# Kernel tuning notes

Measured on AMD Instinct MI355X. Metric: run time of the kernel, lower is better.

## Reference

```python
import jax, jax.numpy as jnp
import numpy as np

TAU = 1.1      # LIF membrane time constant
ALPHA = 4.0    # sigmoid surrogate sharpness (spikingjelly default)
EPS = 1e-5     # BatchNorm eps
SCALE = 0.125  # attention scale


def lif(x, v_th):
    # Single-step LIF, v init 0, decay_input=True: v = x / tau; spike = H(v - v_th)
    # Straight-through: forward heaviside, backward sigmoid surrogate derivative.
    u = x / TAU - v_th
    sg = jax.nn.sigmoid(ALPHA * u)
    return sg + jax.lax.stop_gradient((u >= 0.0).astype(x.dtype) - sg)


def bn(x, gamma, beta):
    # BatchNorm1d in training mode on [B, C, N]: stats over (B, N) per channel
    mean = jnp.mean(x, axis=(0, 2), keepdims=True)
    var = jnp.var(x, axis=(0, 2), keepdims=True)
    return gamma[None, :, None] * (x - mean) * jax.lax.rsqrt(var + EPS) + beta[None, :, None]


def conv1x1(w, x):
    # Conv1d kernel_size=1: pointwise channel mix, x: [B,C,N], w: [O,C]
    return jnp.einsum('oc,bcn->bon', w, x)


def setup_inputs() -> dict:
    key = jax.random.key(0)
    B, C, N = 32, 512, 1024
    ks = jax.random.split(key, 6)
    s = 1.0 / np.sqrt(C)
    inp = {"x": jax.random.normal(ks[0], (B, C, N), jnp.float32)}
    for name, k in zip(["q", "k", "v", "proj"], ks[1:5]):
        inp[name + "_w"] = jax.random.uniform(k, (C, C), jnp.float32, -s, s)
        inp[name + "_gamma"] = jnp.ones((C,), jnp.float32)
        inp[name + "_beta"] = jnp.zeros((C,), jnp.float32)
    inp["proj_b"] = jax.random.uniform(ks[5], (C,), jnp.float32, -s, s)
    return inp


def reference(x, q_w, q_gamma, q_beta, k_w, k_gamma, k_beta, v_w, v_gamma, v_beta,
              proj_w, proj_b, proj_gamma, proj_beta):
    # x: [B, C, N]
    q = lif(bn(conv1x1(q_w, x), q_gamma, q_beta), 1.0)  # [B,C,N] spikes
    k = lif(bn(conv1x1(k_w, x), k_gamma, k_beta), 1.0)
    v = lif(bn(conv1x1(v_w, x), v_gamma, v_beta), 1.0)
    # linear (softmax-free) attention: kv[c,d] = sum_n k[n,c] v[n,d]
    kv = jnp.einsum('bcn,bdn->bcd', k, v)               # [B,C,C]
    attn = jnp.einsum('bcn,bcd->bdn', q, kv) * SCALE    # [B,C,N] (already transposed back)
    attn = lif(attn, 0.5)
    out = conv1x1(proj_w, attn) + proj_b[None, :, None]
    return lif(bn(out, proj_gamma, proj_beta), 1.0)
```

## Files before the change

### kernel.cpp

```cpp
#include <hip/hip_runtime.h>
#include <cstddef>


#define CC 512
#define BB 32
#define NN 1024

typedef __attribute__((ext_vector_type(4))) float v4f;
typedef __attribute__((ext_vector_type(2))) float v2f;
typedef __attribute__((ext_vector_type(4))) int v4i;
typedef __attribute__((ext_vector_type(8))) int v8i;
typedef unsigned char uchar;
typedef unsigned long long ull;

__device__ __forceinline__ uchar f2e4s(float v) {
  const uchar s = (v < 0.f) ? 0x80 : 0x00;
  float a = fabsf(v);
  if (a >= 464.f) return s | 0x7E;
  if (a < 0.015625f) {
    int q = (int)rintf(a * 512.f);
    return s | (uchar)q;
  }
  const int e = (int)((__float_as_uint(a) >> 23) & 0xFF) - 126;
  const float scale = __uint_as_float((unsigned)(4 - e + 127) << 23);
  const int q = (int)rintf(a * scale);
  int code = ((e - 1 + 7) << 3) + (q - 8);
  if (code > 0x7E) code = 0x7E;
  return s | (uchar)code;
}
__device__ __forceinline__ float e42f(uchar b) {
  const int e = (b >> 3) & 15, m = b & 7;
  const float mag = e ? __uint_as_float((unsigned)((e + 120) << 23) | ((unsigned)m << 20))
                      : (float)m * 0.001953125f;
  return (b & 0x80) ? -mag : mag;
}

__device__ __forceinline__ unsigned pk4_fp8(float a0, float a1, float a2, float a3) {
#if __has_builtin(__builtin_amdgcn_cvt_pk_fp8_f32)
  int r = __builtin_amdgcn_cvt_pk_fp8_f32(a0, a1, 0, false);
  r = __builtin_amdgcn_cvt_pk_fp8_f32(a2, a3, r, true);
  return (unsigned)r;
#else
  return (unsigned)f2e4s(a0) | ((unsigned)f2e4s(a1) << 8) |
         ((unsigned)f2e4s(a2) << 16) | ((unsigned)f2e4s(a3) << 24);
#endif
}
__device__ __forceinline__ uchar enc1(float v) {
#if __has_builtin(__builtin_amdgcn_cvt_pk_fp8_f32)
  return (uchar)(__builtin_amdgcn_cvt_pk_fp8_f32(v, v, 0, false) & 0xFF);
#else
  return f2e4s(v);
#endif
}
template <bool HI>
__device__ __forceinline__ v2f dec2(int src) {
#if __has_builtin(__builtin_amdgcn_cvt_pk_f32_fp8)
  return __builtin_amdgcn_cvt_pk_f32_fp8(src, HI);
#else
  v2f r;
  const int s = HI ? (src >> 16) : src;
  r[0] = e42f((uchar)s);
  r[1] = e42f((uchar)(s >> 8));
  return r;
#endif
}

__device__ __forceinline__ void gload16(const void* g, void* l) {
  __builtin_amdgcn_global_load_lds(
      (const __attribute__((address_space(1))) unsigned int*)g,
      (__attribute__((address_space(3))) unsigned int*)l, 16, 0, 0);
}

__device__ __forceinline__ float2 chan_affine(const float* __restrict__ P, int c,
                                              float g, float bt) {
  const float* pc = P + (size_t)c * 16;
  float S = 0.f, Q = 0.f;
#pragma unroll
  for (int t = 0; t < 8; t++) { S += pc[2 * t]; Q += pc[2 * t + 1]; }
  const float mean = S * (1.f / 32768.f);
  const float var = fmaxf(Q * (1.f / 32768.f) - mean * mean, 0.f);
  const float rinv = 1.f / sqrtf(var + 1e-5f);
  const float a = g * rinv;
  return make_float2(a, bt - mean * a);
}

template <int EPI>
__global__ __launch_bounds__(256) void gemm8(const uchar* __restrict__ A,
                                             const uchar* __restrict__ B,
                                             uchar* __restrict__ Cout,
                                             const float* __restrict__ bias,
                                             int M, int N, int K,
                                             long sA, long sB, long sC) {
  __shared__ __align__(16) uchar lds[32768];
  const int b = blockIdx.z;
  const uchar* Ab = A + (size_t)b * sA;
  const uchar* Bb = B + (size_t)b * sB;
  const int m0 = blockIdx.y * 128, n0 = blockIdx.x * 128;
  const int tid = threadIdx.x;
  const int wave = tid >> 6, lane = tid & 63;
  const int lrow = lane & 15, lquad = lane >> 4;
  const int wr = wave >> 1, wc = wave & 1;

  v4f acc[4][4];
#pragma unroll
  for (int i = 0; i < 4; i++)
#pragma unroll
    for (int j = 0; j < 4; j++) acc[i][j] = (v4f)0.f;

  const uchar* gA0 = Ab + (size_t)(m0 + 32 * wave + lrow) * K + lquad * 32;
  const uchar* gA1 = gA0 + (size_t)16 * K;
  const uchar* gB0 = Bb + (size_t)(n0 + 32 * wave + lrow) * K + lquad * 32;
  const uchar* gB1 = gB0 + (size_t)16 * K;
  uchar* lA0 = lds + (2 * wave) * 2048;
  uchar* lA1 = lA0 + 2048;
  uchar* lB0 = lds + 16384 + (2 * wave) * 2048;
  uchar* lB1 = lB0 + 2048;

  for (int k0 = 0; k0 < K; k0 += 128) {
    gload16(gA0, lA0);
    gload16(gA0 + 16, lA0 + 1024);
    gload16(gA1, lA1);
    gload16(gA1 + 16, lA1 + 1024);
    gload16(gB0, lB0);
    gload16(gB0 + 16, lB0 + 1024);
    gload16(gB1, lB1);
    gload16(gB1 + 16, lB1 + 1024);
    gA0 += 128; gA1 += 128; gB0 += 128; gB1 += 128;
    __syncthreads();
    const uchar* ra = lds + (size_t)(4 * wr) * 2048 + 16 * lane;
    const uchar* rb = lds + 16384 + (size_t)(4 * wc) * 2048 + 16 * lane;
    v8i af[4], bf[4];
#pragma unroll
    for (int i = 0; i < 4; i++) {
      const v4i lo = *(const v4i*)(ra + i * 2048);
      const v4i hi = *(const v4i*)(ra + i * 2048 + 1024);
      af[i][0] = lo[0]; af[i][1] = lo[1]; af[i][2] = lo[2]; af[i][3] = lo[3];
      af[i][4] = hi[0]; af[i][5] = hi[1]; af[i][6] = hi[2]; af[i][7] = hi[3];
    }
#pragma unroll
    for (int j = 0; j < 4; j++) {
      const v4i lo = *(const v4i*)(rb + j * 2048);
      const v4i hi = *(const v4i*)(rb + j * 2048 + 1024);
      bf[j][0] = lo[0]; bf[j][1] = lo[1]; bf[j][2] = lo[2]; bf[j][3] = lo[3];
      bf[j][4] = hi[0]; bf[j][5] = hi[1]; bf[j][6] = hi[2]; bf[j][7] = hi[3];
    }
#pragma unroll
    for (int i = 0; i < 4; i++)
#pragma unroll
      for (int j = 0; j < 4; j++)
        acc[i][j] = __builtin_amdgcn_mfma_scale_f32_16x16x128_f8f6f4(
            af[i], bf[j], acc[i][j], 0, 0, 0, 127, 0, 127);
    __syncthreads();
  }

  if (EPI == 3) {
#pragma unroll
    for (int mi = 0; mi < 4; mi++)
#pragma unroll
      for (int r = 0; r < 4; r++) {
        const float bi = bias[m0 + 64 * wr + 16 * mi + lquad * 4 + r];
#pragma unroll
        for (int ni = 0; ni < 4; ni++) acc[mi][ni][r] += bi;
      }
  }

#pragma unroll
  for (int mi = 0; mi < 4; mi++) {
    const int row0 = m0 + 64 * wr + 16 * mi + lquad * 4;
#pragma unroll
    for (int ni = 0; ni < 4; ni++) {
      const int col = n0 + 64 * wc + 16 * ni + lrow;
      uchar* cp = Cout + (size_t)b * sC + (size_t)row0 * N + col;
      if (EPI == 1) {
#pragma unroll
        for (int r = 0; r < 4; r++) {
          const float u = (acc[mi][ni][r] * 0.125f) / 1.1f - 0.5f;
          cp[(size_t)r * N] = (u >= 0.f) ? (uchar)0x38 : (uchar)0;
        }
      } else {
        const unsigned pk = pk4_fp8(acc[mi][ni][0], acc[mi][ni][1],
                                    acc[mi][ni][2], acc[mi][ni][3]);
#pragma unroll
        for (int r = 0; r < 4; r++) cp[(size_t)r * N] = (uchar)(pk >> (8 * r));
      }
    }
  }
}

template <int EPI>
__global__ __launch_bounds__(512, 2) void gemm8p(const uchar* __restrict__ A,
                                                 const uchar* __restrict__ B,
                                                 uchar* __restrict__ Cout,
                                                 const float* __restrict__ bias,
                                                 int M, int N, int K,
                                                 long sA, long sB, long sC) {
  __shared__ __align__(16) uchar lds[131072];
  const int b = blockIdx.z;
  const uchar* Ab = A + (size_t)b * sA;
  const uchar* Bb = B + (size_t)b * sB;
  const int m0 = blockIdx.y * 256, n0 = blockIdx.x * 256;
  const int tid = threadIdx.x;
  const int wave = tid >> 6, lane = tid & 63;
  const int lrow = lane & 15, lquad = lane >> 4;
  const int wr = wave >> 2, wc = wave & 3;

  v4f acc[8][4];
#pragma unroll
  for (int i = 0; i < 8; i++)
#pragma unroll
    for (int j = 0; j < 4; j++) acc[i][j] = (v4f)0.f;

  const uchar* gA0 = Ab + (size_t)(m0 + 32 * wave + lrow) * K + lquad * 32;
  const uchar* gA1 = gA0 + (size_t)16 * K;
  const uchar* gB0 = Bb + (size_t)(n0 + 32 * wave + lrow) * K + lquad * 32;
  const uchar* gB1 = gB0 + (size_t)16 * K;

  const int NT = K >> 7;

#define SSA_STAGE_A(bufi)                                   \
  do {                                                      \
    uchar* la = lds + (bufi) * 65536 + (2 * wave) * 2048;   \
    gload16(gA0, la);                                       \
    gload16(gA0 + 16, la + 1024);                           \
    gload16(gA1, la + 2048);                                \
    gload16(gA1 + 16, la + 3072);                           \
  } while (0)
#define SSA_STAGE_B(bufi)                                   \
  do {                                                      \
    uchar* lb = lds + (bufi) * 65536 + 32768 + (2 * wave) * 2048; \
    gload16(gB0, lb);                                       \
    gload16(gB0 + 16, lb + 1024);                           \
    gload16(gB1, lb + 2048);                                \
    gload16(gB1 + 16, lb + 3072);                           \
  } while (0)

  SSA_STAGE_A(0);
  SSA_STAGE_B(0);
  gA0 += 128; gA1 += 128; gB0 += 128; gB1 += 128;
  asm volatile("s_waitcnt vmcnt(0)" ::: "memory");
  __builtin_amdgcn_s_barrier();

  for (int kt = 0; kt < NT; ++kt) {
    const int cur = kt & 1;
    const int nxt = cur ^ 1;
    const bool more = (kt + 1 < NT);
    const uchar* raA = lds + cur * 65536 + (8 * wr) * 2048 + 16 * lane;
    const uchar* raB = lds + cur * 65536 + 32768 + (4 * wc) * 2048 + 16 * lane;
    v8i bf[4];
#pragma unroll
    for (int p = 0; p < 4; ++p) {
      const uchar* ra = raA + (2 * p) * 2048;
      const v4i a0lo = *(const v4i*)(ra);
      const v4i a0hi = *(const v4i*)(ra + 1024);
      const v4i a1lo = *(const v4i*)(ra + 2048);
      const v4i a1hi = *(const v4i*)(ra + 3072);
      if (p == 0) {
#pragma unroll
        for (int j = 0; j < 4; ++j) {
          const v4i lo = *(const v4i*)(raB + j * 2048);
          const v4i hi = *(const v4i*)(raB + j * 2048 + 1024);
          bf[j][0] = lo[0]; bf[j][1] = lo[1]; bf[j][2] = lo[2]; bf[j][3] = lo[3];
          bf[j][4] = hi[0]; bf[j][5] = hi[1]; bf[j][6] = hi[2]; bf[j][7] = hi[3];
        }
        if (more) SSA_STAGE_A(nxt);
      }
      if (p == 1 && more) {
        SSA_STAGE_B(nxt);
        gA0 += 128; gA1 += 128; gB0 += 128; gB1 += 128;
      }
      __builtin_amdgcn_s_barrier();
      asm volatile("s_waitcnt lgkmcnt(0)" ::: "memory");
      __builtin_amdgcn_sched_barrier(0);
      __builtin_amdgcn_s_setprio(1);
      v8i af0, af1;
      af0[0] = a0lo[0]; af0[1] = a0lo[1]; af0[2] = a0lo[2]; af0[3] = a0lo[3];
      af0[4] = a0hi[0]; af0[5] = a0hi[1]; af0[6] = a0hi[2]; af0[7] = a0hi[3];
      af1[0] = a1lo[0]; af1[1] = a1lo[1]; af1[2] = a1lo[2]; af1[3] = a1lo[3];
      af1[4] = a1hi[0]; af1[5] = a1hi[1]; af1[6] = a1hi[2]; af1[7] = a1hi[3];
#pragma unroll
      for (int j = 0; j < 4; ++j) {
        acc[2 * p][j] = __builtin_amdgcn_mfma_scale_f32_16x16x128_f8f6f4(
            af0, bf[j], acc[2 * p][j], 0, 0, 0, 127, 0, 127);
        acc[2 * p + 1][j] = __builtin_amdgcn_mfma_scale_f32_16x16x128_f8f6f4(
            af1, bf[j], acc[2 * p + 1][j], 0, 0, 0, 127, 0, 127);
      }
      __builtin_amdgcn_s_setprio(0);
      if (p == 3 && more) asm volatile("s_waitcnt vmcnt(0)" ::: "memory");
      __builtin_amdgcn_s_barrier();
    }
  }
#undef SSA_STAGE_A
#undef SSA_STAGE_B

  if (EPI == 3) {
#pragma unroll
    for (int mi = 0; mi < 8; mi++)
#pragma unroll
      for (int r = 0; r < 4; r++) {
        const float bi = bias[m0 + 128 * wr + 16 * mi + lquad * 4 + r];
#pragma unroll
        for (int ni = 0; ni < 4; ni++) acc[mi][ni][r] += bi;
      }
  }

#pragma unroll
  for (int mi = 0; mi < 8; mi++) {
    const int row0 = m0 + 128 * wr + 16 * mi + lquad * 4;
#pragma unroll
    for (int ni = 0; ni < 4; ni++) {
      const int col = n0 + 64 * wc + 16 * ni + lrow;
      uchar* cp = Cout + (size_t)b * sC + (size_t)row0 * N + col;
      if (EPI == 1) {
#pragma unroll
        for (int r = 0; r < 4; r++) {
          const float u = (acc[mi][ni][r] * 0.125f) / 1.1f - 0.5f;
          cp[(size_t)r * N] = (u >= 0.f) ? (uchar)0x38 : (uchar)0;
        }
      } else {
        const unsigned pk = pk4_fp8(acc[mi][ni][0], acc[mi][ni][1],
                                    acc[mi][ni][2], acc[mi][ni][3]);
#pragma unroll
        for (int r = 0; r < 4; r++) cp[(size_t)r * N] = (uchar)(pk >> (8 * r));
      }
    }
  }
}

__global__ __launch_bounds__(256) void stats_part8_k(const uchar* __restrict__ in,
                                                     float* __restrict__ P,
                                                     long bstride) {
  const int part = blockIdx.x, c = blockIdx.y;
  const int tid = threadIdx.x;
  const int bi = part * 4 + (tid >> 6);
  const int lane = tid & 63;
  const uchar* p = in + (size_t)bi * bstride + (size_t)c * 1024 + lane * 16;
  const uint4 u = *(const uint4*)p;
  const int w4[4] = {(int)u.x, (int)u.y, (int)u.z, (int)u.w};
  float s = 0.f, s2 = 0.f;
#pragma unroll
  for (int t = 0; t < 4; t++) {
    const v2f a = dec2<false>(w4[t]);
    const v2f bb = dec2<true>(w4[t]);
    s += (a[0] + a[1]) + (bb[0] + bb[1]);
    s2 += a[0] * a[0] + a[1] * a[1] + bb[0] * bb[0] + bb[1] * bb[1];
  }
#pragma unroll
  for (int off = 32; off > 0; off >>= 1) {
    s += __shfl_down(s, off, 64);
    s2 += __shfl_down(s2, off, 64);
  }
  __shared__ float rs[4], rq[4];
  const int w = tid >> 6;
  if (lane == 0) { rs[w] = s; rq[w] = s2; }
  __syncthreads();
  if (tid == 0) {
    float2 o = make_float2(rs[0] + rs[1] + rs[2] + rs[3],
                           rq[0] + rq[1] + rq[2] + rq[3]);
    *(float2*)(P + (size_t)(c * 8 + part) * 2) = o;
  }
}

__global__ __launch_bounds__(256) void apply_all_k(const uchar* __restrict__ qkv8,
                                                   uchar* __restrict__ q8,
                                                   uchar* __restrict__ k8,
                                                   uchar* __restrict__ v8,
                                                   const float* __restrict__ P,
                                                   const float* __restrict__ qg, const float* __restrict__ qb,
                                                   const float* __restrict__ kg, const float* __restrict__ kb,
                                                   const float* __restrict__ vg, const float* __restrict__ vb) {
  const int bid = blockIdx.x;
  const int tid = threadIdx.x;
  if (bid < 16384) {
    __shared__ uchar tile[32][33];
    const int nb = bid & 31, cb = (bid >> 5) & 15, b = bid >> 9;
    const int n0 = nb * 32, c0 = cb * 32;
    const uchar* in = qkv8 + (size_t)b * (1536 * 1024);
    const int cl = tid >> 3;
    const int n4 = (tid & 7) * 4;
    const int c = c0 + cl;
    const float2 ab = chan_affine(P, c, qg[c], qb[c]);
    const unsigned w = *(const unsigned*)(in + (size_t)c * 1024 + n0 + n4);
    const v2f a = dec2<false>((int)w);
    const v2f bb = dec2<true>((int)w);
    tile[cl][n4 + 0] = (ab.x * a[0] + ab.y >= 1.1f) ? (uchar)0x38 : (uchar)0;
    tile[cl][n4 + 1] = (ab.x * a[1] + ab.y >= 1.1f) ? (uchar)0x38 : (uchar)0;
    tile[cl][n4 + 2] = (ab.x * bb[0] + ab.y >= 1.1f) ? (uchar)0x38 : (uchar)0;
    tile[cl][n4 + 3] = (ab.x * bb[1] + ab.y >= 1.1f) ? (uchar)0x38 : (uchar)0;
    __syncthreads();
    uchar* out = q8 + (size_t)b * (NN * CC);
    const int nl = tid >> 3;
    const int cq = (tid & 7) * 4;
    uchar4 v;
    v.x = tile[cq][nl]; v.y = tile[cq + 1][nl];
    v.z = tile[cq + 2][nl]; v.w = tile[cq + 3][nl];
    *(uchar4*)(out + (size_t)(n0 + nl) * CC + c0 + cq) = v;
  } else {
    const int t0 = bid - 16384;
    const int sec = t0 >> 13;
    const int blk = t0 & 8191;
    const size_t t = (size_t)blk * 256 + tid;
    const size_t i = t * 8;
    const int b = (int)(i >> 19);
    const int rem = (int)(i & 524287);
    const int c = rem >> 10, n = rem & 1023;
    const int cg = 512 + 512 * sec + c;
    const float2 ab = chan_affine(P, cg, sec ? vg[c] : kg[c], sec ? vb[c] : kb[c]);
    const uchar* src = qkv8 + (size_t)b * (1536 * 1024) + (size_t)cg * 1024 + n;
    const uint2 u = *(const uint2*)src;
    ull packed = 0;
    {
      const v2f a = dec2<false>((int)u.x);
      const v2f bb = dec2<true>((int)u.x);
      const float f[4] = {a[0], a[1], bb[0], bb[1]};
#pragma unroll
      for (int j = 0; j < 4; j++)
        packed |= ((ab.x * f[j] + ab.y >= 1.1f) ? 0x38ull : 0ull) << (8 * j);
    }
    {
      const v2f a = dec2<false>((int)u.y);
      const v2f bb = dec2<true>((int)u.y);
      const float f[4] = {a[0], a[1], bb[0], bb[1]};
#pragma unroll
      for (int j = 0; j < 4; j++)
        packed |= ((ab.x * f[j] + ab.y >= 1.1f) ? 0x38ull : 0ull) << (8 * (4 + j));
    }
    uchar* dst = (sec ? v8 : k8) + (size_t)b * (CC * NN) + (size_t)c * 1024 + n;
    *(ull*)dst = packed;
  }
}

__global__ __launch_bounds__(256) void apply_final_k(const uchar* __restrict__ in,
                                                     float* __restrict__ outp,
                                                     const float* __restrict__ Pp,
                                                     const float* __restrict__ pg,
                                                     const float* __restrict__ pb) {
  const size_t idx = ((size_t)blockIdx.x * 256 + threadIdx.x) * 8;
  const int c = (int)((idx >> 10) & (CC - 1));
  const float2 ab = chan_affine(Pp, c, pg[c], pb[c]);
  const uint2 u = *(const uint2*)(in + idx);
  float of[8];
  {
    const v2f a = dec2<false>((int)u.x);
    const v2f bb = dec2<true>((int)u.x);
    of[0] = (ab.x * a[0] + ab.y >= 1.1f) ? 1.f : 0.f;
    of[1] = (ab.x * a[1] + ab.y >= 1.1f) ? 1.f : 0.f;
    of[2] = (ab.x * bb[0] + ab.y >= 1.1f) ? 1.f : 0.f;
    of[3] = (ab.x * bb[1] + ab.y >= 1.1f) ? 1.f : 0.f;
  }
  {
    const v2f a = dec2<false>((int)u.y);
    const v2f bb = dec2<true>((int)u.y);
    of[4] = (ab.x * a[0] + ab.y >= 1.1f) ? 1.f : 0.f;
    of[5] = (ab.x * a[1] + ab.y >= 1.1f) ? 1.f : 0.f;
    of[6] = (ab.x * bb[0] + ab.y >= 1.1f) ? 1.f : 0.f;
    of[7] = (ab.x * bb[1] + ab.y >= 1.1f) ? 1.f : 0.f;
  }
  float* op = outp + idx;
  *(float4*)op = make_float4(of[0], of[1], of[2], of[3]);
  *(float4*)(op + 4) = make_float4(of[4], of[5], of[6], of[7]);
}

__global__ __launch_bounds__(256) void prep_k(const float* __restrict__ x,
                                              const float* __restrict__ w0, const float* __restrict__ w1,
                                              const float* __restrict__ w2, const float* __restrict__ w3,
                                              uchar* __restrict__ xT8,
                                              uchar* __restrict__ o0, uchar* __restrict__ o1,
                                              uchar* __restrict__ o2, uchar* __restrict__ o3) {
  const int bid = blockIdx.x;
  const int tid = threadIdx.x;
  if (bid < 16384) {
    __shared__ uchar tile[32][33];
    const int nb = bid & 31, cb = (bid >> 5) & 15, b = bid >> 9;
    const int n0 = nb * 32, c0 = cb * 32;
    const float* in = x + (size_t)b * (CC * NN);
    const int tx = tid & 31, ty = tid >> 5;
#pragma unroll
    for (int i = 0; i < 32; i += 8) {
      tile[ty + i][tx] = enc1(in[(size_t)(c0 + ty + i) * NN + n0 + tx]);
    }
    __syncthreads();
    uchar* o = xT8 + (size_t)b * (NN * CC);
    const int nl = tid >> 3;
    const int cq = (tid & 7) * 4;
    uchar4 v;
    v.x = tile[cq][nl]; v.y = tile[cq + 1][nl];
    v.z = tile[cq + 2][nl]; v.w = tile[cq + 3][nl];
    *(uchar4*)(o + (size_t)(n0 + nl) * CC + c0 + cq) = v;
  } else {
    const int t = bid - 16384;
    const int mat = t >> 8, blk = t & 255;
    const float* src = (mat == 0) ? w0 : (mat == 1) ? w1 : (mat == 2) ? w2 : w3;
    uchar* dst = (mat == 0) ? o0 : (mat == 1) ? o1 : (mat == 2) ? o2 : o3;
    const int i = (blk * 256 + tid) * 4;
    float4 v = *(const float4*)(src + i);
    *(unsigned*)(dst + i) = pk4_fp8(v.x, v.y, v.z, v.w);
  }
}

extern "C" void kernel_launch(void* const* d_in, const int* in_sizes, int n_in,
                              void* d_out, int out_size, void* d_ws, size_t ws_size,
                              hipStream_t stream) {
  const float* x          = (const float*)d_in[0];
  const float* q_w        = (const float*)d_in[1];
  const float* q_gamma    = (const float*)d_in[2];
  const float* q_beta     = (const float*)d_in[3];
  const float* k_w        = (const float*)d_in[4];
  const float* k_gamma    = (const float*)d_in[5];
  const float* k_beta     = (const float*)d_in[6];
  const float* v_w        = (const float*)d_in[7];
  const float* v_gamma    = (const float*)d_in[8];
  const float* v_beta     = (const float*)d_in[9];
  const float* proj_w     = (const float*)d_in[10];
  const float* proj_gamma = (const float*)d_in[11];
  const float* proj_beta  = (const float*)d_in[12];
  const float* proj_b     = (const float*)d_in[13];

  char* base = (char*)d_ws;
  const size_t MB = 1u << 20;
  uchar*  xT8    = (uchar*)base;
  uchar*  qkv8   = (uchar*)(base + 16 * MB);
  uchar*  q8     = (uchar*)(base + 64 * MB);
  uchar*  k8     = (uchar*)(base + 80 * MB);
  uchar*  v8     = (uchar*)(base + 96 * MB);
  uchar*  kvT8   = (uchar*)(base + 112 * MB);
  uchar*  attnT8 = (uchar*)(base + 120 * MB);
  uchar*  outpre8= (uchar*)(base + 136 * MB);
  uchar*  wqkv8  = (uchar*)(base + 152 * MB);
  uchar*  wp8    = wqkv8 + 3 * CC * CC;
  float*  P      = (float*)(base + 154 * MB);
  float*  Pp     = P + 1536 * 16;
  float* dout = (float*)d_out;

  const long QKVL = (long)3 * CC * NN;
  const long NCL  = (long)NN * CC;
  const long CNL  = (long)CC * NN;
  const long KVL  = (long)CC * CC;

  prep_k<<<17408, 256, 0, stream>>>(x, q_w, k_w, v_w, proj_w, xT8,
                                    wqkv8, wqkv8 + CC * CC, wqkv8 + 2 * CC * CC, wp8);

  gemm8p<2><<<dim3(NN / 256, 1536 / 256, BB), 512, 0, stream>>>(
      wqkv8, xT8, qkv8, nullptr, 1536, NN, CC, 0, NCL, QKVL);

  stats_part8_k<<<dim3(8, 1536), 256, 0, stream>>>(qkv8, P, QKVL);

  apply_all_k<<<32768, 256, 0, stream>>>(qkv8, q8, k8, v8, P,
                                         q_gamma, q_beta, k_gamma, k_beta,
                                         v_gamma, v_beta);

  gemm8<0><<<dim3(CC / 128, CC / 128, BB), 256, 0, stream>>>(
      v8, k8, kvT8, nullptr, CC, CC, NN, CNL, CNL, KVL);
  gemm8p<1><<<dim3(CC / 256, NN / 256, BB), 512, 0, stream>>>(
      q8, kvT8, attnT8, nullptr, NN, CC, CC, NCL, KVL, NCL);
  gemm8p<3><<<dim3(NN / 256, CC / 256, BB), 512, 0, stream>>>(
      wp8, attnT8, outpre8, proj_b, CC, NN, CC, 0, NCL, CNL);

  stats_part8_k<<<dim3(8, CC), 256, 0, stream>>>(outpre8, Pp, CNL);
  apply_final_k<<<8192, 256, 0, stream>>>(outpre8, dout, Pp, proj_gamma, proj_beta);
}
```

Before: 313.1 us.

## Restructure FP8 GEMM main loop to keep two tiles in flight with fewer barriers

The GEMM main loop now issues loads for two K tiles ahead. It waits with a partial vmcnt(8), so the next tile's global->LDS loads stay outstanding while the current tile computes. The per-p-step double barriers and lgkmcnt waits inside the inner loop are removed, leaving one barrier per tile before compute and one before refilling the buffer. This cuts synchronisation overhead and improves load/compute overlap, but removing sched_barrier and the explicit lgkmcnt waits leaves LDS read scheduling to the compiler. The vmcnt counting assumes exactly 8 loads per stage.

```diff
diff --git a/kernel.cpp b/kernel.cpp
--- a/kernel.cpp
+++ b/kernel.cpp
@@ -217,66 +217,55 @@
 
   const int NT = K >> 7;
 
-#define SSA_STAGE_A(bufi)                                   \
-  do {                                                      \
-    uchar* la = lds + (bufi) * 65536 + (2 * wave) * 2048;   \
-    gload16(gA0, la);                                       \
-    gload16(gA0 + 16, la + 1024);                           \
-    gload16(gA1, la + 2048);                                \
-    gload16(gA1 + 16, la + 3072);                           \
-  } while (0)
-#define SSA_STAGE_B(bufi)                                   \
-  do {                                                      \
-    uchar* lb = lds + (bufi) * 65536 + 32768 + (2 * wave) * 2048; \
-    gload16(gB0, lb);                                       \
-    gload16(gB0 + 16, lb + 1024);                           \
-    gload16(gB1, lb + 2048);                                \
-    gload16(gB1 + 16, lb + 3072);                           \
-  } while (0)
-
-  SSA_STAGE_A(0);
-  SSA_STAGE_B(0);
-  gA0 += 128; gA1 += 128; gB0 += 128; gB1 += 128;
-  asm volatile("s_waitcnt vmcnt(0)" ::: "memory");
-  __builtin_amdgcn_s_barrier();
+  auto stage = [&](int bufi) {
+    uchar* la = lds + bufi * 65536 + (2 * wave) * 2048;
+    uchar* lb = la + 32768;
+    gload16(gA0, la);
+    gload16(gA0 + 16, la + 1024);
+    gload16(gA1, la + 2048);
+    gload16(gA1 + 16, la + 3072);
+    gload16(gB0, lb);
+    gload16(gB0 + 16, lb + 1024);
+    gload16(gB1, lb + 2048);
+    gload16(gB1 + 16, lb + 3072);
+    gA0 += 128; gA1 += 128; gB0 += 128; gB1 += 128;
+  };
+
+  stage(0);
+  if (NT > 1) stage(1);
 
   for (int kt = 0; kt < NT; ++kt) {
     const int cur = kt & 1;
-    const int nxt = cur ^ 1;
-    const bool more = (kt + 1 < NT);
-    const uchar* raA = lds + cur * 65536 + (8 * wr) * 2048 + 16 * lane;
-    const uchar* raB = lds + cur * 65536 + 32768 + (4 * wc) * 2048 + 16 * lane;
+    if (kt + 1 < NT) {
+      asm volatile("s_waitcnt vmcnt(8)" ::: "memory");
+    } else {
+      asm volatile("s_waitcnt vmcnt(0)" ::: "memory");
+    }
+    __builtin_amdgcn_s_barrier();
+
+    const uchar* raA = lds + cur * 65536 + (size_t)(8 * wr) * 2048 + 16 * lane;
+    const uchar* raB = lds + cur * 65536 + 32768 + (size_t)(4 * wc) * 2048 + 16 * lane;
     v8i bf[4];
 #pragma unroll
+    for (int j = 0; j < 4; ++j) {
+      const v4i lo = *(const v4i*)(raB + j * 2048);
+      const v4i hi = *(const v4i*)(raB + j * 2048 + 1024);
+      bf[j][0] = lo[0]; bf[j][1] = lo[1]; bf[j][2] = lo[2]; bf[j][3] = lo[3];
+      bf[j][4] = hi[0]; bf[j][5] = hi[1]; bf[j][6] = hi[2]; bf[j][7] = hi[3];
+    }
+#pragma unroll
     for (int p = 0; p < 4; ++p) {
-      const uchar* ra = raA + (2 * p) * 2048;
+      const uchar* ra = raA + (size_t)(2 * p) * 2048;
       const v4i a0lo = *(const v4i*)(ra);
       const v4i a0hi = *(const v4i*)(ra + 1024);
       const v4i a1lo = *(const v4i*)(ra + 2048);
       const v4i a1hi = *(const v4i*)(ra + 3072);
-      if (p == 0) {
-#pragma unroll
-        for (int j = 0; j < 4; ++j) {
-          const v4i lo = *(const v4i*)(raB + j * 2048);
-          const v4i hi = *(const v4i*)(raB + j * 2048 + 1024);
-          bf[j][0] = lo[0]; bf[j][1] = lo[1]; bf[j][2] = lo[2]; bf[j][3] = lo[3];
-          bf[j][4] = hi[0]; bf[j][5] = hi[1]; bf[j][6] = hi[2]; bf[j][7] = hi[3];
-        }
-        if (more) SSA_STAGE_A(nxt);
-      }
-      if (p == 1 && more) {
-        SSA_STAGE_B(nxt);
-        gA0 += 128; gA1 += 128; gB0 += 128; gB1 += 128;
-      }
-      __builtin_amdgcn_s_barrier();
-      asm volatile("s_waitcnt lgkmcnt(0)" ::: "memory");
-      __builtin_amdgcn_sched_barrier(0);
-      __builtin_amdgcn_s_setprio(1);
       v8i af0, af1;
       af0[0] = a0lo[0]; af0[1] = a0lo[1]; af0[2] = a0lo[2]; af0[3] = a0lo[3];
       af0[4] = a0hi[0]; af0[5] = a0hi[1]; af0[6] = a0hi[2]; af0[7] = a0hi[3];
       af1[0] = a1lo[0]; af1[1] = a1lo[1]; af1[2] = a1lo[2]; af1[3] = a1lo[3];
       af1[4] = a1hi[0]; af1[5] = a1hi[1]; af1[6] = a1hi[2]; af1[7] = a1hi[3];
+      __builtin_amdgcn_s_setprio(1);
 #pragma unroll
       for (int j = 0; j < 4; ++j) {
         acc[2 * p][j] = __builtin_amdgcn_mfma_scale_f32_16x16x128_f8f6f4(
@@ -285,12 +274,13 @@
             af1, bf[j], acc[2 * p + 1][j], 0, 0, 0, 127, 0, 127);
       }
       __builtin_amdgcn_s_setprio(0);
-      if (p == 3 && more) asm volatile("s_waitcnt vmcnt(0)" ::: "memory");
+    }
+
+    if (kt + 2 < NT) {
       __builtin_amdgcn_s_barrier();
-    }
-  }
-#undef SSA_STAGE_A
-#undef SSA_STAGE_B
+      stage(cur);
+    }
+  }
 
   if (EPI == 3) {
 #pragma unroll
```

Result: faster. 299.4 us (-4.4%).
